# Kernel tuning notes

Hardware: AMD Instinct MI355X
Metric: run time of the kernel (lower is better)

The kernel has to match this reference:

```python
import jax, jax.numpy as jnp
import numpy as np
import math


def sinusoidal_embedding(n_pos, d_model, dtype=jnp.float32):
    # matches SpaceEmbedding: se[:,0::2]=sin(pos*div), se[:,1::2]=cos(pos*div)
    pos = jnp.arange(n_pos, dtype=dtype)[:, None]                      # [T,1]
    div = jnp.exp(jnp.arange(0, d_model, 2, dtype=dtype) * (-math.log(10000.0) / d_model))  # [d/2]
    ang = pos * div                                                    # [T,d/2]
    se = jnp.stack([jnp.sin(ang), jnp.cos(ang)], axis=-1).reshape(n_pos, d_model)
    return se


def setup_inputs() -> dict:
    key = jax.random.key(0)
    ks = jax.random.split(key, 6)
    B, D_in, T, d = 32, 512, 1024, 1024
    s_in = 1.0 / np.sqrt(D_in)
    s_d = 1.0 / np.sqrt(d)
    return {
        "xs": jax.random.normal(ks[0], (B, D_in, T), dtype=jnp.float32),
        "W_embed": jax.random.uniform(ks[1], (d, D_in), minval=-s_in, maxval=s_in, dtype=jnp.float32),
        "W_KQ": jax.random.uniform(ks[2], (d, d), minval=-s_d, maxval=s_d, dtype=jnp.float32),
        "W_PV": jax.random.uniform(ks[3], (d, d), minval=-s_d, maxval=s_d, dtype=jnp.float32),
        "W_un": jax.random.uniform(ks[4], (D_in, d), minval=-s_d, maxval=s_d, dtype=jnp.float32),
        "b_un": jnp.zeros((D_in,), dtype=jnp.float32),
    }


def reference(xs, W_embed, W_KQ, W_PV, W_un, b_un):
    B, D_in, T = xs.shape
    d = W_embed.shape[0]
    rho = 1.0
    # patch embedding: Linear(dim_input, d_model, bias=False) on [B,T,D_in]
    patch = jnp.einsum('bnt,dn->btd', xs, W_embed)                     # [B,T,d]
    emb = patch + sinusoidal_embedding(T, d, patch.dtype)[None]        # [B,T,d]
    E = jnp.transpose(emb, (0, 2, 1))                                  # [B,d,T]
    X = E[:, :, :-1]                                                   # [B,d,T-1] (skip last token)
    # attn_arg = X^T @ W_KQ @ E / rho  -> [B,T-1,T]
    attn_arg = jnp.einsum('bdm,de,bet->bmt', X, W_KQ, E) / rho
    soft = jax.nn.softmax(attn_arg, axis=1)                            # softmax over T-1 (keys) dim
    # f_attn = W_PV @ X @ soft -> [B,d,T]
    f_attn = jnp.einsum('de,bem,bmt->bdt', W_PV, X, soft)
    # unembed: Linear(d_model, dim_input) applied to [B,T,d], then transpose back
    out_full = jnp.einsum('bdt,od->bot', f_attn, W_un) + b_un[None, :, None]  # [B,D_in,T]
    return out_full, attn_arg
```

## Files before the change

### kernel.cpp

```cpp
#include <hip/hip_runtime.h>
#include <hip/hip_bf16.h>
#include <cstdio>

typedef __bf16 bf16;
typedef __bf16 bf16x4 __attribute__((ext_vector_type(4)));
typedef __bf16 bf16x8 __attribute__((ext_vector_type(8)));
typedef float  f32x4  __attribute__((ext_vector_type(4)));

#define AS1 __attribute__((address_space(1)))
#define AS3 __attribute__((address_space(3)))

__device__ __forceinline__ void async16(void* lds, const void* g) {
    __builtin_amdgcn_global_load_lds((AS1 unsigned int*)g, (AS3 unsigned int*)lds, 16, 0, 0);
}

enum { EPI_NONE = 0, EPI_SINUS = 1, EPI_BIAS = 2, EPI_ATTN = 3 };

#define FENCE asm volatile("" ::: "memory")
#define BAR   do { FENCE; __builtin_amdgcn_s_barrier(); FENCE; } while (0)
#define LGKM0 asm volatile("s_waitcnt lgkmcnt(0)" ::: "memory")
#define RD8(p) (*(const bf16x8*)(const void*)(p))

#define MFMA_Q(AF, MB, BF, NB)                                                 \
    _Pragma("unroll") for (int mf = 0; mf < 4; ++mf)                           \
    _Pragma("unroll") for (int nf = 0; nf < 2; ++nf)                           \
    _Pragma("unroll") for (int s = 0; s < 2; ++s)                              \
        acc[(MB) + mf][(NB) + nf] = __builtin_amdgcn_mfma_f32_16x16x32_bf16(   \
            AF[mf][s], BF[nf][s], acc[(MB) + mf][(NB) + nf], 0, 0, 0);

__device__ __forceinline__ void onl_merge(float& mx, float& sm, float omx, float osm) {
    float nm = fmaxf(mx, omx);
    sm = sm * __expf(mx - nm) + osm * __expf(omx - nm);
    mx = nm;
}

template <int EPI, typename CT>
__launch_bounds__(512, 2)
__global__ void gemm8(const bf16* __restrict__ A, long sA, int lda,
                      const bf16* __restrict__ B, long sB, int ldb,
                      CT* __restrict__ C, long sC, int ldc,
                      int K, int mLimit, const float* __restrict__ bias,
                      float* __restrict__ pmx, float* __restrict__ psum,
                      int tilesM, int tilesN)
{
    __shared__ __align__(16) char smem[131072];
    char* ldsA = smem;
    char* ldsB = smem + 65536;

    const int tid  = threadIdx.x;
    const int wave = tid >> 6;
    const int lane = tid & 63;
    const int quad = lane >> 4;
    const int l16  = lane & 15;
    const int hw   = wave >> 2;
    const int wq   = wave & 3;
    const int hbB  = wq >> 1;
    const int rrB  = (wq & 1) * 64;

    const int nwg = gridDim.x;
    const int qq = nwg >> 3, rr = nwg & 7;
    const int xcd = blockIdx.x & 7, idx = blockIdx.x >> 3;
    const int wgid = (xcd < rr ? xcd * (qq + 1) : rr * (qq + 1) + (xcd - rr) * qq) + idx;

    const int tpb = tilesM * tilesN;
    const int b   = wgid / tpb;
    const int rem = wgid - b * tpb;
    const int m0  = (rem / tilesN) * 256;
    const int n0  = (rem % tilesN) * 256;

    A += (long)b * sA;
    B += (long)b * sB;

    const int odt  = wave * 1024 + lane * 16;
    const int ol   = odt ^ (((odt >> 7) & 7) << 4);
    const int srow = ol >> 7;
    const int scol = (ol & 127) >> 1;
    const bf16* pA = A + (long)(m0 + srow) * lda + scol;
    const bf16* pB = B + (long)(n0 + srow) * ldb + scol;

    const int xr = (l16 & 7) << 4;
    const int lane2_0 = ((l16 * 128) + (quad * 16)) ^ xr;
    const int lane2_1 = ((l16 * 128) + 64 + (quad * 16)) ^ xr;

    auto stgA = [&](int bb, int h, int kt) {
        char* l = ldsA + bb * 32768 + h * 16384 + wave * 1024;
        const bf16* g = pA + (long)(h * 128) * lda + kt * 64;
        async16(l, g);
        async16(l + 8192, g + (long)64 * lda);
    };
    auto stgB = [&](int bb, int h, int kt) {
        char* l = ldsB + bb * 32768 + h * 16384 + wave * 1024;
        const bf16* g = pB + (long)(h * 128) * ldb + kt * 64;
        async16(l, g);
        async16(l + 8192, g + (long)64 * ldb);
    };

    const int nk = K >> 6;

    stgA(0, 0, 0); stgA(0, 1, 0);
    stgB(0, 0, 0); stgB(0, 1, 0);
    stgA(1, 0, 1); stgA(1, 1, 1);
    asm volatile("s_waitcnt vmcnt(4)" ::: "memory");
    BAR;

    f32x4 acc[8][4] = {};

    for (int t = 0; t < nk; ++t) {
        const int cur = t & 1;
        const char* aH = ldsA + cur * 32768 + hw * 16384;
        const char* bH = ldsB + cur * 32768 + hbB * 16384 + rrB * 128;

        bf16x8 af03[4][2], af47[4][2], bf01[2][2], bf23[2][2];

        #pragma unroll
        for (int mf = 0; mf < 4; ++mf) {
            af03[mf][0] = RD8(aH + mf * 2048 + lane2_0);
            af03[mf][1] = RD8(aH + mf * 2048 + lane2_1);
        }
        #pragma unroll
        for (int nf = 0; nf < 2; ++nf) {
            bf01[nf][0] = RD8(bH + nf * 2048 + lane2_0);
            bf01[nf][1] = RD8(bH + nf * 2048 + lane2_1);
        }
        if (t + 1 < nk) stgB(cur ^ 1, 0, t + 1);
        BAR;
        LGKM0;
        __builtin_amdgcn_s_setprio(1);
        MFMA_Q(af03, 0, bf01, 0);
        __builtin_amdgcn_s_setprio(0);
        BAR;

        #pragma unroll
        for (int nf = 0; nf < 2; ++nf) {
            bf23[nf][0] = RD8(bH + (nf + 2) * 2048 + lane2_0);
            bf23[nf][1] = RD8(bH + (nf + 2) * 2048 + lane2_1);
        }
        if (t + 1 < nk) stgB(cur ^ 1, 1, t + 1);
        BAR;
        LGKM0;
        __builtin_amdgcn_s_setprio(1);
        MFMA_Q(af03, 0, bf23, 2);
        __builtin_amdgcn_s_setprio(0);
        BAR;

        #pragma unroll
        for (int mf = 0; mf < 4; ++mf) {
            af47[mf][0] = RD8(aH + (mf + 4) * 2048 + lane2_0);
            af47[mf][1] = RD8(aH + (mf + 4) * 2048 + lane2_1);
        }
        if (t + 2 < nk) stgA(cur, 0, t + 2);
        BAR;
        LGKM0;
        __builtin_amdgcn_s_setprio(1);
        MFMA_Q(af47, 4, bf01, 0);
        __builtin_amdgcn_s_setprio(0);
        BAR;

        if (t + 2 < nk) {
            stgA(cur, 1, t + 2);
            asm volatile("s_waitcnt vmcnt(4)" ::: "memory");
        } else {
            asm volatile("s_waitcnt vmcnt(0)" ::: "memory");
        }
        BAR;
        __builtin_amdgcn_s_setprio(1);
        MFMA_Q(af47, 4, bf23, 2);
        __builtin_amdgcn_s_setprio(0);
        BAR;
    }

    C += (long)b * sC;

    #pragma unroll
    for (int nf = 0; nf < 4; ++nf) {
        const int col = n0 + wq * 64 + nf * 16 + l16;
        float fr = 0.f;
        if (EPI == EPI_SINUS)
            fr = __expf((float)(-(col & ~1)) * (9.210340371976184f / 1024.f));
        #pragma unroll
        for (int mf = 0; mf < 8; ++mf) {
            #pragma unroll
            for (int r = 0; r < 4; ++r) {
                const int row = m0 + hw * 128 + mf * 16 + quad * 4 + r;
                float v = acc[mf][nf][r];
                if (EPI == EPI_SINUS) {
                    float ang = (float)row * fr;
                    v += (col & 1) ? __cosf(ang) : __sinf(ang);
                }
                if (EPI == EPI_BIAS) v += bias[row];
                if (row < mLimit)
                    C[(long)row * ldc + col] = (CT)v;
            }
        }
    }

    if (EPI == EPI_ATTN) {
        float nmx[4], nsm[4];
        #pragma unroll
        for (int nf = 0; nf < 4; ++nf) {
            float mx = -1e30f;
            #pragma unroll
            for (int mf = 0; mf < 8; ++mf)
                #pragma unroll
                for (int r = 0; r < 4; ++r) {
                    const int row = m0 + hw * 128 + mf * 16 + quad * 4 + r;
                    float v = (row < mLimit) ? acc[mf][nf][r] : -1e30f;
                    mx = fmaxf(mx, v);
                }
            float sm = 0.f;
            #pragma unroll
            for (int mf = 0; mf < 8; ++mf)
                #pragma unroll
                for (int r = 0; r < 4; ++r) {
                    const int row = m0 + hw * 128 + mf * 16 + quad * 4 + r;
                    float v = (row < mLimit) ? acc[mf][nf][r] : -1e30f;
                    sm += __expf(v - mx);
                }
            float omx = __shfl_xor(mx, 16), osm = __shfl_xor(sm, 16);
            onl_merge(mx, sm, omx, osm);
            omx = __shfl_xor(mx, 32); osm = __shfl_xor(sm, 32);
            onl_merge(mx, sm, omx, osm);
            nmx[nf] = mx; nsm[nf] = sm;
        }
        float smx = quad == 0 ? nmx[0] : quad == 1 ? nmx[1] : quad == 2 ? nmx[2] : nmx[3];
        float ssm = quad == 0 ? nsm[0] : quad == 1 ? nsm[1] : quad == 2 ? nsm[2] : nsm[3];
        float2* red = (float2*)smem;
        red[wave * 64 + lane] = make_float2(smx, ssm);
        __syncthreads();
        if (wave < 4) {
            float2 x = red[wave * 64 + lane];
            float2 y = red[(wave + 4) * 64 + lane];
            onl_merge(x.x, x.y, y.x, y.y);
            const int col = n0 + wq * 64 + lane;
            const int mt  = m0 >> 8;
            pmx [((long)b * 4 + mt) * 1024 + col] = x.x;
            psum[((long)b * 4 + mt) * 1024 + col] = x.y;
        }
    }
}

constexpr int BM = 128, BN = 128, BK = 32;
template <int EPI, typename CT>
__launch_bounds__(256)
__global__ void gemm_nt(const bf16* __restrict__ A, long sA, int lda,
                        const bf16* __restrict__ B, long sB, int ldb,
                        CT* __restrict__ C, long sC, int ldc,
                        int K, int mLimit,
                        const float* __restrict__ bias)
{
    __shared__ __align__(16) bf16 As[BM * BK];
    __shared__ __align__(16) bf16 Bs[BN * BK];

    const int tid  = threadIdx.x;
    const int wave = tid >> 6;
    const int lane = tid & 63;
    const int quad = lane >> 4;
    const int l16  = lane & 15;
    const int b    = blockIdx.z;
    const int m0   = blockIdx.y * BM;
    const int n0   = blockIdx.x * BN;

    A += (long)b * sA;
    B += (long)b * sB;

    const int srow = lane >> 2;
    const int scol = (lane & 3) * 8;
    const bf16* gA = A + (long)(m0 + wave * 32 + srow) * lda + scol;
    const bf16* gB = B + (long)(n0 + wave * 32 + srow) * ldb + scol;
    char* lA = (char*)As + wave * 2048;
    char* lB = (char*)Bs + wave * 2048;

    const int wm = (wave >> 1) * 64;
    const int wn = (wave & 1) * 64;

    f32x4 acc[4][4] = {};

    for (int k0 = 0; k0 < K; k0 += BK) {
        __syncthreads();
        async16(lA,        gA);
        async16(lA + 1024, gA + (long)16 * lda);
        async16(lB,        gB);
        async16(lB + 1024, gB + (long)16 * ldb);
        gA += BK; gB += BK;
        __syncthreads();

        bf16x8 af[4], bfr[4];
        #pragma unroll
        for (int i = 0; i < 4; i++) {
            af[i]  = *(const bf16x8*)(As + (wm + i * 16 + l16) * BK + quad * 8);
            bfr[i] = *(const bf16x8*)(Bs + (wn + i * 16 + l16) * BK + quad * 8);
        }
        #pragma unroll
        for (int mi = 0; mi < 4; mi++)
            #pragma unroll
            for (int ni = 0; ni < 4; ni++)
                acc[mi][ni] = __builtin_amdgcn_mfma_f32_16x16x32_bf16(
                    af[mi], bfr[ni], acc[mi][ni], 0, 0, 0);
    }

    C += (long)b * sC;

    #pragma unroll
    for (int ni = 0; ni < 4; ni++) {
        const int col = n0 + wn + ni * 16 + l16;
        #pragma unroll
        for (int mi = 0; mi < 4; mi++) {
            #pragma unroll
            for (int r = 0; r < 4; r++) {
                const int row = m0 + wm + mi * 16 + quad * 4 + r;
                float v = acc[mi][ni][r];
                if (EPI == EPI_BIAS) v += bias[row];
                if (row < mLimit)
                    C[(long)row * ldc + col] = (CT)v;
            }
        }
    }
}

__launch_bounds__(256)
__global__ void cvt_f32_bf16(const float* __restrict__ in, bf16* __restrict__ out, int n)
{
    int i = (blockIdx.x * 256 + threadIdx.x) * 4;
    if (i < n) {
        float4 v = *(const float4*)(in + i);
        out[i]     = (bf16)v.x;
        out[i + 1] = (bf16)v.y;
        out[i + 2] = (bf16)v.z;
        out[i + 3] = (bf16)v.w;
    }
}

__launch_bounds__(256)
__global__ void transpose_f32_bf16(const float* __restrict__ in, bf16* __restrict__ out,
                                   int rows, int cols)
{
    __shared__ float tile[32][33];
    const long bs = (long)rows * cols;
    in  += (long)blockIdx.z * bs;
    out += (long)blockIdx.z * bs;
    const int c0 = blockIdx.x * 32, r0 = blockIdx.y * 32;
    const int tx = threadIdx.x, ty = threadIdx.y;
    #pragma unroll
    for (int i = ty; i < 32; i += 8)
        tile[i][tx] = in[(long)(r0 + i) * cols + c0 + tx];
    __syncthreads();
    #pragma unroll
    for (int i = ty; i < 32; i += 8)
        out[(long)(c0 + i) * rows + r0 + tx] = (bf16)tile[tx][i];
}

__launch_bounds__(256)
__global__ void transpose_bf16(const bf16* __restrict__ in, bf16* __restrict__ out,
                               int rows, int cols)
{
    __shared__ bf16 tile[32][33];
    const long bs = (long)rows * cols;
    in  += (long)blockIdx.z * bs;
    out += (long)blockIdx.z * bs;
    const int c0 = blockIdx.x * 32, r0 = blockIdx.y * 32;
    const int tx = threadIdx.x, ty = threadIdx.y;
    #pragma unroll
    for (int i = ty; i < 32; i += 8)
        tile[i][tx] = in[(long)(r0 + i) * cols + c0 + tx];
    __syncthreads();
    #pragma unroll
    for (int i = ty; i < 32; i += 8)
        out[(long)(c0 + i) * rows + r0 + tx] = tile[tx][i];
}

__launch_bounds__(256)
__global__ void softmax_norm_T(const float* __restrict__ attn,
                               const float* __restrict__ pmx,
                               const float* __restrict__ psum,
                               bf16* __restrict__ softT)
{
    __shared__ bf16 tile[64][66];
    const int b  = blockIdx.z;
    const int mt = blockIdx.x;
    const int ct = blockIdx.y;
    const int tx = threadIdx.x & 63;
    const int ty = threadIdx.x >> 6;
    const int col = ct * 64 + tx;

    float MX = -1e30f, SM = 0.f;
    #pragma unroll
    for (int p = 0; p < 4; ++p) {
        float omx = pmx [((long)b * 4 + p) * 1024 + col];
        float osm = psum[((long)b * 4 + p) * 1024 + col];
        onl_merge(MX, SM, omx, osm);
    }
    const float INV = 1.f / SM;

    const float* a = attn + (long)b * (1023l * 1024);
    const int m0 = mt * 64;
    #pragma unroll
    for (int i = ty; i < 64; i += 4) {
        const int m = m0 + i;
        float p = 0.f;
        if (m < 1023) p = __expf(a[(long)m * 1024 + col] - MX) * INV;
        tile[tx][i] = (bf16)p;
    }
    __syncthreads();
    bf16* o = softT + (long)b * (1024l * 1024) + (long)(ct * 64) * 1024 + m0;
    #pragma unroll
    for (int j = ty; j < 64; j += 4)
        o[(long)j * 1024 + tx] = tile[j][tx];
}

extern "C" void kernel_launch(void* const* d_in, const int* in_sizes, int n_in,
                              void* d_out, int out_size, void* d_ws, size_t ws_size,
                              hipStream_t stream)
{
    const float* xs    = (const float*)d_in[0];
    const float* W_emb = (const float*)d_in[1];
    const float* W_KQ  = (const float*)d_in[2];
    const float* W_PV  = (const float*)d_in[3];
    const float* W_un  = (const float*)d_in[4];
    const float* b_un  = (const float*)d_in[5];

    float* out  = (float*)d_out;
    float* attn = out + (size_t)32 * 512 * 1024;

    const long MB = 1024l * 1024;

    char* ws = (char*)d_ws;
    const size_t oXsT  = 0;
    const size_t oET   = oXsT + (size_t)33554432;
    const size_t oEn   = oET  + (size_t)67108864;
    const size_t oQT   = oEn  + (size_t)67108864;
    const size_t oR    = oQT  + (size_t)67108864;
    const size_t oWe   = oR   + (size_t)67108864;
    const size_t oWkq  = oWe  + (size_t)1048576;
    const size_t oWpvT = oWkq + (size_t)2097152;
    const size_t oWun  = oWpvT + (size_t)2097152;
    const size_t oWc   = oWun + (size_t)1048576;
    const size_t need  = oWc  + (size_t)1048576;
    if (ws_size < need) { fprintf(stderr, "ws too small: %zu < %zu\n", ws_size, need); return; }

    bf16* xsT   = (bf16*)(ws + oXsT);
    bf16* ET    = (bf16*)(ws + oET);
    bf16* En    = (bf16*)(ws + oEn);
    bf16* QT    = (bf16*)(ws + oQT);
    bf16* We    = (bf16*)(ws + oWe);
    bf16* Wkq   = (bf16*)(ws + oWkq);
    bf16* WpvT  = (bf16*)(ws + oWpvT);
    bf16* Wun   = (bf16*)(ws + oWun);
    bf16* Wc    = (bf16*)(ws + oWc);
    bf16* softT = QT;
    bf16* A1T   = (bf16*)(ws + oR);

    float* pmx  = (float*)(ws + oR);
    float* psum = pmx + (size_t)32 * 4 * 1024;

    const dim3 tb(32, 8);
    const int BIG = 1 << 30;

    cvt_f32_bf16<<<512, 256, 0, stream>>>(W_emb, We, 524288);
    cvt_f32_bf16<<<1024, 256, 0, stream>>>(W_KQ, Wkq, 1048576);
    cvt_f32_bf16<<<512, 256, 0, stream>>>(W_un, Wun, 524288);
    transpose_f32_bf16<<<dim3(32, 32, 1), tb, 0, stream>>>(W_PV, WpvT, 1024, 1024);
    gemm_nt<EPI_NONE, bf16><<<dim3(8, 4, 1), 256, 0, stream>>>(
        Wun, 0, 1024, WpvT, 0, 1024, Wc, 0, 1024, 1024, BIG, nullptr);
    transpose_f32_bf16<<<dim3(32, 16, 32), tb, 0, stream>>>(xs, xsT, 512, 1024);
    gemm8<EPI_SINUS, bf16><<<dim3(512), 512, 0, stream>>>(
        xsT, 512l * 1024, 512, We, 0, 512, ET, MB, 1024, 512, BIG, nullptr, nullptr, nullptr, 4, 4);
    transpose_bf16<<<dim3(32, 32, 32), tb, 0, stream>>>(ET, En, 1024, 1024);
    gemm8<EPI_NONE, bf16><<<dim3(512), 512, 0, stream>>>(
        ET, MB, 1024, Wkq, 0, 1024, QT, MB, 1024, 1024, BIG, nullptr, nullptr, nullptr, 4, 4);
    gemm8<EPI_ATTN, float><<<dim3(512), 512, 0, stream>>>(
        ET, MB, 1024, QT, MB, 1024, attn, 1023l * 1024, 1024, 1024, 1023, nullptr, pmx, psum, 4, 4);
    softmax_norm_T<<<dim3(16, 16, 32), 256, 0, stream>>>(attn, pmx, psum, softT);
    gemm8<EPI_NONE, bf16><<<dim3(512), 512, 0, stream>>>(
        softT, MB, 1024, En, MB, 1024, A1T, MB, 1024, 1024, BIG, nullptr, nullptr, nullptr, 4, 4);
    gemm8<EPI_BIAS, float><<<dim3(256), 512, 0, stream>>>(
        Wc, 0, 1024, A1T, MB, 1024, out, 512l * 1024, 1024, 1024, BIG, b_un, nullptr, nullptr, 2, 4);
}
```

Before: 744.5 us.

## Software-pipeline LDS fragment reads across GEMM k-iterations with partial lgkmcnt waits

Restructures the GEMM main loop so LDS fragment loads for the next k-tile (af03, bf01) are issued before the last MFMA quadrant of the current iteration. Intermediate fragment loads are issued ahead of the MFMA that does not need them, using partial lgkmcnt waits. This removes several barriers per iteration and lets LDS reads overlap with matrix-core work. The two A-tile global-to-LDS stages are merged into the final phase. The risk is a read/write race on the double-buffered LDS tiles if the remaining barriers and vmcnt waits do not cover the reordered async writes.

```diff
diff --git a/kernel.cpp b/kernel.cpp
--- a/kernel.cpp
+++ b/kernel.cpp
@@ -18,7 +18,7 @@
 
 #define FENCE asm volatile("" ::: "memory")
 #define BAR   do { FENCE; __builtin_amdgcn_s_barrier(); FENCE; } while (0)
-#define LGKM0 asm volatile("s_waitcnt lgkmcnt(0)" ::: "memory")
+#define LGKMC(n) asm volatile("s_waitcnt lgkmcnt(" #n ")" ::: "memory")
 #define RD8(p) (*(const bf16x8*)(const void*)(p))
 
 #define MFMA_Q(AF, MB, BF, NB)                                                 \
@@ -104,14 +104,11 @@
     BAR;
 
     f32x4 acc[8][4] = {};
-
-    for (int t = 0; t < nk; ++t) {
-        const int cur = t & 1;
-        const char* aH = ldsA + cur * 32768 + hw * 16384;
-        const char* bH = ldsB + cur * 32768 + hbB * 16384 + rrB * 128;
-
-        bf16x8 af03[4][2], af47[4][2], bf01[2][2], bf23[2][2];
-
+    bf16x8 af03[4][2], af47[4][2], bf01[2][2], bf23[2][2];
+
+    {
+        const char* aH = ldsA + hw * 16384;
+        const char* bH = ldsB + hbB * 16384 + rrB * 128;
         #pragma unroll
         for (int mf = 0; mf < 4; ++mf) {
             af03[mf][0] = RD8(aH + mf * 2048 + lane2_0);
@@ -122,47 +119,65 @@
             bf01[nf][0] = RD8(bH + nf * 2048 + lane2_0);
             bf01[nf][1] = RD8(bH + nf * 2048 + lane2_1);
         }
+    }
+
+    for (int t = 0; t < nk; ++t) {
+        const int cur = t & 1;
+        const char* aH  = ldsA + cur * 32768 + hw * 16384;
+        const char* bH  = ldsB + cur * 32768 + hbB * 16384 + rrB * 128;
+        const char* aHn = ldsA + (cur ^ 1) * 32768 + hw * 16384;
+        const char* bHn = ldsB + (cur ^ 1) * 32768 + hbB * 16384 + rrB * 128;
+
+        #pragma unroll
+        for (int nf = 0; nf < 2; ++nf) {
+            bf23[nf][0] = RD8(bH + (nf + 2) * 2048 + lane2_0);
+            bf23[nf][1] = RD8(bH + (nf + 2) * 2048 + lane2_1);
+        }
         if (t + 1 < nk) stgB(cur ^ 1, 0, t + 1);
-        BAR;
-        LGKM0;
+        LGKMC(4);
         __builtin_amdgcn_s_setprio(1);
         MFMA_Q(af03, 0, bf01, 0);
         __builtin_amdgcn_s_setprio(0);
         BAR;
 
         #pragma unroll
-        for (int nf = 0; nf < 2; ++nf) {
-            bf23[nf][0] = RD8(bH + (nf + 2) * 2048 + lane2_0);
-            bf23[nf][1] = RD8(bH + (nf + 2) * 2048 + lane2_1);
+        for (int mf = 0; mf < 4; ++mf) {
+            af47[mf][0] = RD8(aH + (mf + 4) * 2048 + lane2_0);
+            af47[mf][1] = RD8(aH + (mf + 4) * 2048 + lane2_1);
         }
         if (t + 1 < nk) stgB(cur ^ 1, 1, t + 1);
-        BAR;
-        LGKM0;
+        LGKMC(8);
         __builtin_amdgcn_s_setprio(1);
         MFMA_Q(af03, 0, bf23, 2);
         __builtin_amdgcn_s_setprio(0);
         BAR;
 
-        #pragma unroll
-        for (int mf = 0; mf < 4; ++mf) {
-            af47[mf][0] = RD8(aH + (mf + 4) * 2048 + lane2_0);
-            af47[mf][1] = RD8(aH + (mf + 4) * 2048 + lane2_1);
-        }
-        if (t + 2 < nk) stgA(cur, 0, t + 2);
-        BAR;
-        LGKM0;
+        LGKMC(0);
         __builtin_amdgcn_s_setprio(1);
         MFMA_Q(af47, 4, bf01, 0);
         __builtin_amdgcn_s_setprio(0);
         BAR;
 
         if (t + 2 < nk) {
+            stgA(cur, 0, t + 2);
             stgA(cur, 1, t + 2);
             asm volatile("s_waitcnt vmcnt(4)" ::: "memory");
         } else {
             asm volatile("s_waitcnt vmcnt(0)" ::: "memory");
         }
         BAR;
+        if (t + 1 < nk) {
+            #pragma unroll
+            for (int mf = 0; mf < 4; ++mf) {
+                af03[mf][0] = RD8(aHn + mf * 2048 + lane2_0);
+                af03[mf][1] = RD8(aHn + mf * 2048 + lane2_1);
+            }
+            #pragma unroll
+            for (int nf = 0; nf < 2; ++nf) {
+                bf01[nf][0] = RD8(bHn + nf * 2048 + lane2_0);
+                bf01[nf][1] = RD8(bHn + nf * 2048 + lane2_1);
+            }
+        }
         __builtin_amdgcn_s_setprio(1);
         MFMA_Q(af47, 4, bf23, 2);
         __builtin_amdgcn_s_setprio(0);
```

Measured after the change: 755.1 us. About the same (+1.4%).
